# Optimization experiments

Measured on AMD Instinct MI355X. Metric: run time of the kernel, lower is better.

Reference implementation:

```python
import jax, jax.numpy as jnp
import numpy as np

INPUT_DIM = 1024
CODEBOOK_DIM = 128
CODEBOOK_SIZE = 8192
B, N = 8, 4096


def setup_inputs() -> dict:
    key = jax.random.key(0)
    k1, k2, k3 = jax.random.split(key, 3)
    x = jax.random.normal(k1, (B, N, INPUT_DIM), dtype=jnp.float32)
    # xavier_normal_: std = sqrt(2 / (fan_in + fan_out))
    xavier_std = float(np.sqrt(2.0 / (INPUT_DIM + CODEBOOK_DIM)))
    random_projection = jax.random.normal(k2, (INPUT_DIM, CODEBOOK_DIM), dtype=jnp.float32) * xavier_std
    codebook = jax.random.normal(k3, (CODEBOOK_SIZE, CODEBOOK_DIM), dtype=jnp.float32)
    return {"x": x, "random_projection": random_projection, "codebook": codebook}


def reference(x, random_projection, codebook):
    # random projection: [B, N, D] @ [D, E] -> [B, N, E]
    proj = jnp.einsum("bnd,de->bne", x, random_projection)
    b, n, e = proj.shape
    flat = proj.reshape(b * n, e)  # [BN, E]
    eps = 1e-12  # matches torch F.normalize default eps
    nx = flat / jnp.maximum(jnp.linalg.norm(flat, axis=1, keepdims=True), eps)
    ncb = codebook / jnp.maximum(jnp.linalg.norm(codebook, axis=1, keepdims=True), eps)
    # squared euclidean distances [K, BN]; argmin of d^2 == argmin of cdist
    d2 = (
        jnp.sum(ncb * ncb, axis=1)[:, None]
        + jnp.sum(nx * nx, axis=1)[None, :]
        - 2.0 * (ncb @ nx.T)
    )
    nearest = jnp.argmin(d2, axis=0)  # [BN]
    return nearest.reshape(b, n).astype(jnp.int32)
```

## Files before the change

kernel.cpp:

```cpp
#include <hip/hip_runtime.h>
#include <math.h>
#include <float.h>
#include <limits.h>

#define BN      32768
#define D_IN    1024
#define E_DIM   128
#define CB_N    8192

typedef _Float16 f16x8 __attribute__((ext_vector_type(8)));
typedef _Float16 f16x4 __attribute__((ext_vector_type(4)));
typedef float    f32x4 __attribute__((ext_vector_type(4)));

#define GLL16(gsrc, ldst)                                                      \
    __builtin_amdgcn_global_load_lds(                                          \
        (const __attribute__((address_space(1))) unsigned int*)(const void*)(gsrc), \
        (__attribute__((address_space(3))) unsigned int*)(void*)(ldst), 16, 0, 0)


__global__ __launch_bounds__(256) void pack_all_kernel(
    const float* __restrict__ cb, _Float16* __restrict__ ph,
    _Float16* __restrict__ pl,
    const float* __restrict__ rp, _Float16* __restrict__ rph,
    _Float16* __restrict__ rpl) {
    __shared__ float L[16][129];
    __shared__ float R[32][132];
    const int t = threadIdx.x;
    const int b = blockIdx.x;

    if (b < 512) {
        const int g = b;
        const int c = t >> 4, p = t & 15;
        const float4 v0 = *(const float4*)&cb[(size_t)(g * 16 + c) * E_DIM + p * 8];
        const float4 v1 = *(const float4*)&cb[(size_t)(g * 16 + c) * E_DIM + p * 8 + 4];
        float ss = v0.x * v0.x + v0.y * v0.y + v0.z * v0.z + v0.w * v0.w
                 + v1.x * v1.x + v1.y * v1.y + v1.z * v1.z + v1.w * v1.w;
#pragma unroll
        for (int m = 1; m < 16; m <<= 1) ss += __shfl_xor(ss, m);
        const float inv = 256.0f / fmaxf(sqrtf(ss), 1e-12f);

        L[c][p * 8 + 0] = v0.x * inv; L[c][p * 8 + 1] = v0.y * inv;
        L[c][p * 8 + 2] = v0.z * inv; L[c][p * 8 + 3] = v0.w * inv;
        L[c][p * 8 + 4] = v1.x * inv; L[c][p * 8 + 5] = v1.y * inv;
        L[c][p * 8 + 6] = v1.z * inv; L[c][p * 8 + 7] = v1.w * inv;
        __syncthreads();

        const int kb = t >> 6, lane = t & 63;
        const int quad = (lane >> 4), col = lane & 15;
        f16x8 h, l;
#pragma unroll
        for (int j = 0; j < 8; ++j) {
            const float v = L[col][kb * 32 + quad * 8 + j];
            const _Float16 hv = (_Float16)v;
            h[j] = hv;
            l[j] = (_Float16)(v - (float)hv);
        }
        const size_t off = ((size_t)(g * 4 + kb) * 64 + lane) * 8;
        *(f16x8*)&ph[off] = h;
        *(f16x8*)&pl[off] = l;
    } else {
        const int kb = b - 512;
        const int r = t >> 3, c0 = (t & 7) * 16;
#pragma unroll
        for (int i = 0; i < 4; ++i)
            *(float4*)&R[r][c0 + i * 4] =
                *(const float4*)&rp[(size_t)(kb * 32 + r) * E_DIM + c0 + i * 4];
        __syncthreads();

        const int w = t >> 6, lane = t & 63;
        const int quad = lane >> 4, col = lane & 15;
#pragma unroll
        for (int h2 = 0; h2 < 2; ++h2) {
            const int nt = w * 2 + h2;
            f16x8 hh, ll;
#pragma unroll
            for (int j = 0; j < 8; ++j) {
                const float v = R[quad * 8 + j][nt * 16 + col] * 64.0f;
                const _Float16 hv = (_Float16)v;
                hh[j] = hv;
                ll[j] = (_Float16)(v - (float)hv);
            }
            const size_t off = ((size_t)((kb * 8 + nt) * 64) + lane) * 8;
            *(f16x8*)&rph[off] = hh;
            *(f16x8*)&rpl[off] = ll;
        }
    }
}

#define PPITCH   132
#define P_BYTES  (128 * PPITCH * 4)
#define CH_BYTES 32768
#define NCHUNK   128

__global__ __launch_bounds__(512, 2) void fused_kernel(
    const float* __restrict__ x,
    const _Float16* __restrict__ rph, const _Float16* __restrict__ rpl,
    const _Float16* __restrict__ ph, const _Float16* __restrict__ pl,
    int* __restrict__ out) {
    __shared__ __align__(16) char SMEM[P_BYTES];

    const int tid  = threadIdx.x;
    const int lane = tid & 63;
    const int w    = tid >> 6;
    const int quad = lane >> 4, col = lane & 15;
    const int qb   = blockIdx.x * 128;

    float* Pf  = (float*)SMEM;
    char*  Bst = SMEM;

    const int wn  = w & 3;
    const int wq1 = w >> 2;
    const int qbw = qb + wq1 * 64;

    const float* xr[4];
#pragma unroll
    for (int mt = 0; mt < 4; ++mt)
        xr[mt] = x + (size_t)(qbw + mt * 16 + col) * D_IN + quad * 8;

    f32x4 acc[4][2];
#pragma unroll
    for (int mt = 0; mt < 4; ++mt)
#pragma unroll
        for (int h = 0; h < 2; ++h) acc[mt][h] = (f32x4){0.f, 0.f, 0.f, 0.f};

    float4 pA[4][2];
#pragma unroll
    for (int mt = 0; mt < 4; ++mt) {
        pA[mt][0] = *(const float4*)(xr[mt] + 0);
        pA[mt][1] = *(const float4*)(xr[mt] + 4);
    }
    f16x8 bhc[2], blc[2];
#pragma unroll
    for (int h = 0; h < 2; ++h) {
        const size_t off = ((size_t)(wn * 2 + h) * 64 + lane) * 8;
        bhc[h] = *(const f16x8*)&rph[off];
        blc[h] = *(const f16x8*)&rpl[off];
    }

    for (int kb = 0; kb < 32; ++kb) {
        f16x8 ah1[4], al1[4];
#pragma unroll
        for (int mt = 0; mt < 4; ++mt) {
            const float vv[8] = {pA[mt][0].x, pA[mt][0].y, pA[mt][0].z, pA[mt][0].w,
                                 pA[mt][1].x, pA[mt][1].y, pA[mt][1].z, pA[mt][1].w};
            f16x8 hh, ll;
#pragma unroll
            for (int j = 0; j < 8; ++j) {
                const float v = vv[j] * 512.0f;
                const _Float16 hv = (_Float16)v;
                hh[j] = hv;
                ll[j] = (_Float16)(v - (float)hv);
            }
            ah1[mt] = hh;
            al1[mt] = ll;
        }

        if (kb + 1 < 32) {
#pragma unroll
            for (int mt = 0; mt < 4; ++mt) {
                pA[mt][0] = *(const float4*)(xr[mt] + (kb + 1) * 32);
                pA[mt][1] = *(const float4*)(xr[mt] + (kb + 1) * 32 + 4);
            }
        }

        f16x8 bh1[2] = {bhc[0], bhc[1]};
        f16x8 bl1[2] = {blc[0], blc[1]};
        if (kb + 1 < 32) {
#pragma unroll
            for (int h = 0; h < 2; ++h) {
                const size_t off = ((size_t)((kb + 1) * 8 + wn * 2 + h) * 64 + lane) * 8;
                bhc[h] = *(const f16x8*)&rph[off];
                blc[h] = *(const f16x8*)&rpl[off];
            }
        }

#pragma unroll
        for (int mt = 0; mt < 4; ++mt)
#pragma unroll
            for (int h = 0; h < 2; ++h)
                acc[mt][h] = __builtin_amdgcn_mfma_f32_16x16x32_f16(ah1[mt], bh1[h], acc[mt][h], 0, 0, 0);
#pragma unroll
        for (int mt = 0; mt < 4; ++mt)
#pragma unroll
            for (int h = 0; h < 2; ++h)
                acc[mt][h] = __builtin_amdgcn_mfma_f32_16x16x32_f16(ah1[mt], bl1[h], acc[mt][h], 0, 0, 0);
#pragma unroll
        for (int mt = 0; mt < 4; ++mt)
#pragma unroll
            for (int h = 0; h < 2; ++h)
                acc[mt][h] = __builtin_amdgcn_mfma_f32_16x16x32_f16(al1[mt], bh1[h], acc[mt][h], 0, 0, 0);
    }

#pragma unroll
    for (int mt = 0; mt < 4; ++mt)
#pragma unroll
        for (int h = 0; h < 2; ++h)
#pragma unroll
            for (int r = 0; r < 4; ++r) {
                const int row = wq1 * 64 + mt * 16 + quad * 4 + r;
                const int cc  = wn * 32 + h * 16 + col;
                Pf[row * PPITCH + cc] = acc[mt][h][r] * (1.0f / 2048.0f);
            }
    __syncthreads();

    f16x8 ah[4], al[4];
#pragma unroll
    for (int kb = 0; kb < 4; ++kb) {
        const int base = (w * 16 + col) * PPITCH + kb * 32 + quad * 8;
        const float4 v0 = *(const float4*)&Pf[base];
        const float4 v1 = *(const float4*)&Pf[base + 4];
        const float vv[8] = {v0.x, v0.y, v0.z, v0.w, v1.x, v1.y, v1.z, v1.w};
        f16x8 hh, ll;
#pragma unroll
        for (int j = 0; j < 8; ++j) {
            const _Float16 hv = (_Float16)vv[j];
            hh[j] = hv;
            ll[j] = (_Float16)(vv[j] - (float)hv);
        }
        ah[kb] = hh;
        al[kb] = ll;
    }
    __syncthreads();

    const char* const sb[2] = {(const char*)ph, (const char*)pl};
    int sti[4], ssel[4], skb[4];
#pragma unroll
    for (int i = 0; i < 4; ++i) {
        const int idx = w * 4 + i;
        sti[i] = idx >> 3; ssel[i] = (idx >> 2) & 1; skb[i] = idx & 3;
    }

#pragma unroll
    for (int i = 0; i < 4; ++i) {
        const char* g = sb[ssel[i]] + (size_t)((0 + sti[i]) * 4 + skb[i]) * 1024 + (size_t)lane * 16;
        char* l = Bst + sti[i] * 8192 + ssel[i] * 4096 + skb[i] * 1024;
        GLL16(g, l);
    }
    __syncthreads();

    float bs[4];
    int   bi[4];
#pragma unroll
    for (int s = 0; s < 4; ++s) { bs[s] = -FLT_MAX; bi[s] = 0; }

    for (int c = 0; c < NCHUNK; ++c) {
        const int cur = c & 1;
        if (c + 1 < NCHUNK) {
            const int nxt = cur ^ 1;
#pragma unroll
            for (int i = 0; i < 4; ++i) {
                const char* g = sb[ssel[i]] + (size_t)(((c + 1) * 4 + sti[i]) * 4 + skb[i]) * 1024 + (size_t)lane * 16;
                char* l = Bst + nxt * CH_BYTES + sti[i] * 8192 + ssel[i] * 4096 + skb[i] * 1024;
                GLL16(g, l);
            }
        }

        const char* bb = Bst + cur * CH_BYTES + (size_t)lane * 16;
#pragma unroll
        for (int p = 0; p < 2; ++p) {
            f16x8 bhA[4], blA[4], bhB[4], blB[4];
#pragma unroll
            for (int kb = 0; kb < 4; ++kb) {
                bhA[kb] = *(const f16x8*)(bb + (p * 2 + 0) * 8192 + kb * 1024);
                blA[kb] = *(const f16x8*)(bb + (p * 2 + 0) * 8192 + 4096 + kb * 1024);
                bhB[kb] = *(const f16x8*)(bb + (p * 2 + 1) * 8192 + kb * 1024);
                blB[kb] = *(const f16x8*)(bb + (p * 2 + 1) * 8192 + 4096 + kb * 1024);
            }

            f32x4 sA = (f32x4){0.f, 0.f, 0.f, 0.f};
            f32x4 sB = (f32x4){0.f, 0.f, 0.f, 0.f};

            __builtin_amdgcn_s_setprio(1);
#pragma unroll
            for (int kb = 0; kb < 4; ++kb) {
                sA = __builtin_amdgcn_mfma_f32_16x16x32_f16(ah[kb], bhA[kb], sA, 0, 0, 0);
                sB = __builtin_amdgcn_mfma_f32_16x16x32_f16(ah[kb], bhB[kb], sB, 0, 0, 0);
            }
#pragma unroll
            for (int kb = 0; kb < 4; ++kb) {
                sA = __builtin_amdgcn_mfma_f32_16x16x32_f16(ah[kb], blA[kb], sA, 0, 0, 0);
                sB = __builtin_amdgcn_mfma_f32_16x16x32_f16(ah[kb], blB[kb], sB, 0, 0, 0);
            }
#pragma unroll
            for (int kb = 0; kb < 4; ++kb) {
                sA = __builtin_amdgcn_mfma_f32_16x16x32_f16(al[kb], bhA[kb], sA, 0, 0, 0);
                sB = __builtin_amdgcn_mfma_f32_16x16x32_f16(al[kb], bhB[kb], sB, 0, 0, 0);
            }
            __builtin_amdgcn_s_setprio(0);

            const int codeA = c * 64 + (p * 2 + 0) * 16 + col;
            const int codeB = c * 64 + (p * 2 + 1) * 16 + col;
#pragma unroll
            for (int r = 0; r < 4; ++r) {
                if (sA[r] > bs[r]) { bs[r] = sA[r]; bi[r] = codeA; }
            }
#pragma unroll
            for (int r = 0; r < 4; ++r) {
                if (sB[r] > bs[r]) { bs[r] = sB[r]; bi[r] = codeB; }
            }
        }

        if (c + 1 < NCHUNK) __syncthreads();
    }

#pragma unroll
    for (int s = 0; s < 4; ++s) {
#pragma unroll
        for (int m = 1; m < 16; m <<= 1) {
            const float os = __shfl_xor(bs[s], m);
            const int   oi = __shfl_xor(bi[s], m);
            if (os > bs[s] || (os == bs[s] && oi < bi[s])) { bs[s] = os; bi[s] = oi; }
        }
    }

    if (col == 0) {
#pragma unroll
        for (int r = 0; r < 4; ++r)
            out[qb + w * 16 + quad * 4 + r] = bi[r];
    }
}

extern "C" void kernel_launch(void* const* d_in, const int* in_sizes, int n_in,
                              void* d_out, int out_size, void* d_ws, size_t ws_size,
                              hipStream_t stream) {
    const float* x  = (const float*)d_in[0];
    const float* rp = (const float*)d_in[1];
    const float* cb = (const float*)d_in[2];
    int* out = (int*)d_out;

    _Float16* ph  = (_Float16*)d_ws;
    _Float16* pl  = ph  + (size_t)CB_N * E_DIM;
    _Float16* rph = pl  + (size_t)CB_N * E_DIM;
    _Float16* rpl = rph + (size_t)D_IN * E_DIM;

    pack_all_kernel<<<CB_N / 16 + 32, 256, 0, stream>>>(cb, ph, pl, rp, rph, rpl);
    fused_kernel<<<BN / 128, 512, 0, stream>>>(x, rph, rpl, ph, pl, out);
}
```

Baseline: 407.3 us.

## Retile codebook search so each wave covers two query tiles and half the codebook

Each wave now holds A fragments for two 16-query tiles and scans one half of the codebook, instead of one query tile against the whole codebook. Every B fragment loaded from LDS is reused across two query tiles, halving LDS read traffic per MFMA. The codebook staging layout changes so each half is streamed by the waves that own it, and a final cross-wave merge through shared memory combines the two halves' argmax results. This doubles the A-fragment and best-score register footprint and adds a small LDS reduction step. Tie-breaking across halves favours the lower-index half, so it matches the reference's first-minimum choice.

```diff
diff --git a/kernel.cpp b/kernel.cpp
--- a/kernel.cpp
+++ b/kernel.cpp
@@ -98,6 +98,8 @@
     const _Float16* __restrict__ ph, const _Float16* __restrict__ pl,
     int* __restrict__ out) {
     __shared__ __align__(16) char SMEM[P_BYTES];
+    __shared__ float ls[8][32];
+    __shared__ int   li[8][32];
 
     const int tid  = threadIdx.x;
     const int lane = tid & 63;
@@ -203,45 +205,51 @@
             }
     __syncthreads();
 
-    f16x8 ah[4], al[4];
-#pragma unroll
-    for (int kb = 0; kb < 4; ++kb) {
-        const int base = (w * 16 + col) * PPITCH + kb * 32 + quad * 8;
-        const float4 v0 = *(const float4*)&Pf[base];
-        const float4 v1 = *(const float4*)&Pf[base + 4];
-        const float vv[8] = {v0.x, v0.y, v0.z, v0.w, v1.x, v1.y, v1.z, v1.w};
-        f16x8 hh, ll;
-#pragma unroll
-        for (int j = 0; j < 8; ++j) {
-            const _Float16 hv = (_Float16)vv[j];
-            hh[j] = hv;
-            ll[j] = (_Float16)(vv[j] - (float)hv);
-        }
-        ah[kb] = hh;
-        al[kb] = ll;
-    }
+    const int wq = w >> 1;
+    const int wc = w & 1;
+
+    f16x8 ah[2][4], al[2][4];
+#pragma unroll
+    for (int mt2 = 0; mt2 < 2; ++mt2)
+#pragma unroll
+        for (int kb = 0; kb < 4; ++kb) {
+            const int base = ((wq * 2 + mt2) * 16 + col) * PPITCH + kb * 32 + quad * 8;
+            const float4 v0 = *(const float4*)&Pf[base];
+            const float4 v1 = *(const float4*)&Pf[base + 4];
+            const float vv[8] = {v0.x, v0.y, v0.z, v0.w, v1.x, v1.y, v1.z, v1.w};
+            f16x8 hh, ll;
+#pragma unroll
+            for (int j = 0; j < 8; ++j) {
+                const _Float16 hv = (_Float16)vv[j];
+                hh[j] = hv;
+                ll[j] = (_Float16)(vv[j] - (float)hv);
+            }
+            ah[mt2][kb] = hh;
+            al[mt2][kb] = ll;
+        }
     __syncthreads();
 
     const char* const sb[2] = {(const char*)ph, (const char*)pl};
-    int sti[4], ssel[4], skb[4];
+    int sh2[4], stt[4], ssel[4], skb[4];
 #pragma unroll
     for (int i = 0; i < 4; ++i) {
         const int idx = w * 4 + i;
-        sti[i] = idx >> 3; ssel[i] = (idx >> 2) & 1; skb[i] = idx & 3;
+        sh2[i] = idx >> 4; stt[i] = (idx >> 3) & 1; ssel[i] = (idx >> 2) & 1; skb[i] = idx & 3;
     }
 
 #pragma unroll
     for (int i = 0; i < 4; ++i) {
-        const char* g = sb[ssel[i]] + (size_t)((0 + sti[i]) * 4 + skb[i]) * 1024 + (size_t)lane * 16;
-        char* l = Bst + sti[i] * 8192 + ssel[i] * 4096 + skb[i] * 1024;
+        const int G = sh2[i] * 256 + 0 * 2 + stt[i];
+        const char* g = sb[ssel[i]] + (size_t)(G * 4 + skb[i]) * 1024 + (size_t)lane * 16;
+        char* l = Bst + (w * 4 + i) * 1024;
         GLL16(g, l);
     }
     __syncthreads();
 
-    float bs[4];
-    int   bi[4];
-#pragma unroll
-    for (int s = 0; s < 4; ++s) { bs[s] = -FLT_MAX; bi[s] = 0; }
+    float bs[8];
+    int   bi[8];
+#pragma unroll
+    for (int s = 0; s < 8; ++s) { bs[s] = -FLT_MAX; bi[s] = 0; }
 
     for (int c = 0; c < NCHUNK; ++c) {
         const int cur = c & 1;
@@ -249,54 +257,52 @@
             const int nxt = cur ^ 1;
 #pragma unroll
             for (int i = 0; i < 4; ++i) {
-                const char* g = sb[ssel[i]] + (size_t)(((c + 1) * 4 + sti[i]) * 4 + skb[i]) * 1024 + (size_t)lane * 16;
-                char* l = Bst + nxt * CH_BYTES + sti[i] * 8192 + ssel[i] * 4096 + skb[i] * 1024;
+                const int G = sh2[i] * 256 + (c + 1) * 2 + stt[i];
+                const char* g = sb[ssel[i]] + (size_t)(G * 4 + skb[i]) * 1024 + (size_t)lane * 16;
+                char* l = Bst + nxt * CH_BYTES + (w * 4 + i) * 1024;
                 GLL16(g, l);
             }
         }
 
-        const char* bb = Bst + cur * CH_BYTES + (size_t)lane * 16;
-#pragma unroll
-        for (int p = 0; p < 2; ++p) {
-            f16x8 bhA[4], blA[4], bhB[4], blB[4];
+        const char* bb = Bst + cur * CH_BYTES + wc * 16384 + (size_t)lane * 16;
+#pragma unroll
+        for (int tt = 0; tt < 2; ++tt) {
+            f16x8 bh2[4], bl2[4];
 #pragma unroll
             for (int kb = 0; kb < 4; ++kb) {
-                bhA[kb] = *(const f16x8*)(bb + (p * 2 + 0) * 8192 + kb * 1024);
-                blA[kb] = *(const f16x8*)(bb + (p * 2 + 0) * 8192 + 4096 + kb * 1024);
-                bhB[kb] = *(const f16x8*)(bb + (p * 2 + 1) * 8192 + kb * 1024);
-                blB[kb] = *(const f16x8*)(bb + (p * 2 + 1) * 8192 + 4096 + kb * 1024);
-            }
-
-            f32x4 sA = (f32x4){0.f, 0.f, 0.f, 0.f};
-            f32x4 sB = (f32x4){0.f, 0.f, 0.f, 0.f};
+                bh2[kb] = *(const f16x8*)(bb + tt * 8192 + kb * 1024);
+                bl2[kb] = *(const f16x8*)(bb + tt * 8192 + 4096 + kb * 1024);
+            }
+
+            f32x4 s0 = (f32x4){0.f, 0.f, 0.f, 0.f};
+            f32x4 s1 = (f32x4){0.f, 0.f, 0.f, 0.f};
 
             __builtin_amdgcn_s_setprio(1);
 #pragma unroll
             for (int kb = 0; kb < 4; ++kb) {
-                sA = __builtin_amdgcn_mfma_f32_16x16x32_f16(ah[kb], bhA[kb], sA, 0, 0, 0);
-                sB = __builtin_amdgcn_mfma_f32_16x16x32_f16(ah[kb], bhB[kb], sB, 0, 0, 0);
+                s0 = __builtin_amdgcn_mfma_f32_16x16x32_f16(ah[0][kb], bh2[kb], s0, 0, 0, 0);
+                s1 = __builtin_amdgcn_mfma_f32_16x16x32_f16(ah[1][kb], bh2[kb], s1, 0, 0, 0);
             }
 #pragma unroll
             for (int kb = 0; kb < 4; ++kb) {
-                sA = __builtin_amdgcn_mfma_f32_16x16x32_f16(ah[kb], blA[kb], sA, 0, 0, 0);
-                sB = __builtin_amdgcn_mfma_f32_16x16x32_f16(ah[kb], blB[kb], sB, 0, 0, 0);
+                s0 = __builtin_amdgcn_mfma_f32_16x16x32_f16(ah[0][kb], bl2[kb], s0, 0, 0, 0);
+                s1 = __builtin_amdgcn_mfma_f32_16x16x32_f16(ah[1][kb], bl2[kb], s1, 0, 0, 0);
             }
 #pragma unroll
             for (int kb = 0; kb < 4; ++kb) {
-                sA = __builtin_amdgcn_mfma_f32_16x16x32_f16(al[kb], bhA[kb], sA, 0, 0, 0);
-                sB = __builtin_amdgcn_mfma_f32_16x16x32_f16(al[kb], bhB[kb], sB, 0, 0, 0);
+                s0 = __builtin_amdgcn_mfma_f32_16x16x32_f16(al[0][kb], bh2[kb], s0, 0, 0, 0);
+                s1 = __builtin_amdgcn_mfma_f32_16x16x32_f16(al[1][kb], bh2[kb], s1, 0, 0, 0);
             }
             __builtin_amdgcn_s_setprio(0);
 
-            const int codeA = c * 64 + (p * 2 + 0) * 16 + col;
-            const int codeB = c * 64 + (p * 2 + 1) * 16 + col;
+            const int code = wc * 4096 + c * 32 + tt * 16 + col;
 #pragma unroll
             for (int r = 0; r < 4; ++r) {
-                if (sA[r] > bs[r]) { bs[r] = sA[r]; bi[r] = codeA; }
+                if (s0[r] > bs[r]) { bs[r] = s0[r]; bi[r] = code; }
             }
 #pragma unroll
             for (int r = 0; r < 4; ++r) {
-                if (sB[r] > bs[r]) { bs[r] = sB[r]; bi[r] = codeB; }
+                if (s1[r] > bs[4 + r]) { bs[4 + r] = s1[r]; bi[4 + r] = code; }
             }
         }
 
@@ -304,7 +310,7 @@
     }
 
 #pragma unroll
-    for (int s = 0; s < 4; ++s) {
+    for (int s = 0; s < 8; ++s) {
 #pragma unroll
         for (int m = 1; m < 16; m <<= 1) {
             const float os = __shfl_xor(bs[s], m);
@@ -315,8 +321,24 @@
 
     if (col == 0) {
 #pragma unroll
-        for (int r = 0; r < 4; ++r)
-            out[qb + w * 16 + quad * 4 + r] = bi[r];
+        for (int mt2 = 0; mt2 < 2; ++mt2)
+#pragma unroll
+            for (int r = 0; r < 4; ++r) {
+                ls[w][mt2 * 16 + quad * 4 + r] = bs[mt2 * 4 + r];
+                li[w][mt2 * 16 + quad * 4 + r] = bi[mt2 * 4 + r];
+            }
+    }
+    __syncthreads();
+
+    if (tid < 128) {
+        const int q   = tid;
+        const int wqf = q >> 5;
+        const int q32 = q & 31;
+        float s = ls[wqf * 2 + 0][q32];
+        int   i = li[wqf * 2 + 0][q32];
+        const float os = ls[wqf * 2 + 1][q32];
+        if (os > s) { s = os; i = li[wqf * 2 + 1][q32]; }
+        out[qb + q] = i;
     }
 }
 
```

New measurement: 409.2 us. About the same (+0.5%).
